# Performance work log

Hardware: AMD Instinct MI355X
Metric: run time of the kernel (lower is better)

The kernel has to match this reference:

```python
import jax, jax.numpy as jnp
import numpy as np

N_NODES = 100000
N_EDGES = 1600000
IN_FEAT = 256
OUT_FEAT = 128


def setup_inputs() -> dict:
    key = jax.random.key(0)
    ks = jax.random.split(key, 8)
    x = jax.random.normal(ks[0], (N_NODES, IN_FEAT), dtype=jnp.float32)
    rows0 = jnp.sort(jax.random.randint(ks[1], (N_EDGES,), 0, N_NODES, dtype=jnp.int32))
    cols0 = jax.random.randint(ks[2], (N_EDGES,), 0, N_NODES, dtype=jnp.int32)
    vals0 = jax.random.uniform(ks[3], (N_EDGES,), dtype=jnp.float32)
    rows1 = jnp.sort(jax.random.randint(ks[4], (N_EDGES,), 0, N_NODES, dtype=jnp.int32))
    cols1 = jax.random.randint(ks[5], (N_EDGES,), 0, N_NODES, dtype=jnp.int32)
    vals1 = jax.random.uniform(ks[6], (N_EDGES,), dtype=jnp.float32)
    kw0, kw1 = jax.random.split(ks[7])
    # glorot-uniform-ish scale for [IN_FEAT, OUT_FEAT]
    limit = float(np.sqrt(6.0 / (IN_FEAT + OUT_FEAT)))
    W0 = jax.random.uniform(kw0, (IN_FEAT, OUT_FEAT), minval=-limit, maxval=limit, dtype=jnp.float32)
    W1 = jax.random.uniform(kw1, (IN_FEAT, OUT_FEAT), minval=-limit, maxval=limit, dtype=jnp.float32)
    return {"x": x, "rows0": rows0, "cols0": cols0, "vals0": vals0,
            "rows1": rows1, "cols1": cols1, "vals1": vals1, "W0": W0, "W1": W1}


def _spmm(rows, cols, vals, dense, n_rows):
    # sparse [N,N] (COO) @ dense [N,D] -> [N,D]
    gathered = vals[:, None] * dense[cols]          # [E, D]
    return jax.ops.segment_sum(gathered, rows, num_segments=n_rows)


def reference(x, rows0, cols0, vals0, rows1, cols1, vals1, W0, W1):
    # GraphConvolution with dropout=0 (identity), featureless=False, no bias, relu.
    # support_i = A_i @ (x @ W_i); output = relu(sum_i support_i)
    s0 = _spmm(rows0, cols0, vals0, x @ W0, N_NODES)
    s1 = _spmm(rows1, cols1, vals1, x @ W1, N_NODES)
    return jax.nn.relu(s0 + s1)
```

## Files before the change

kernel.cpp:

```cpp
#include <hip/hip_runtime.h>
#include <hip/hip_bf16.h>
#include <stdint.h>

#define NN   100000
#define NE   1600000
#define KIN  256
#define FOUT 128

typedef __attribute__((ext_vector_type(8))) short short8;
typedef __attribute__((ext_vector_type(4))) float f32x4;
typedef __attribute__((ext_vector_type(2))) float f32x2;

static __device__ __forceinline__ unsigned short f2bf(float f) {
  unsigned int u = __float_as_uint(f);
  u += 0x7fffu + ((u >> 16) & 1u);
  return (unsigned short)(u >> 16);
}

static __device__ __forceinline__ short8 pack8(float4 u, float4 v) {
  short8 r;
  r[0] = (short)f2bf(u.x); r[1] = (short)f2bf(u.y);
  r[2] = (short)f2bf(u.z); r[3] = (short)f2bf(u.w);
  r[4] = (short)f2bf(v.x); r[5] = (short)f2bf(v.y);
  r[6] = (short)f2bf(v.z); r[7] = (short)f2bf(v.w);
  return r;
}

__global__ void convert_w(const float* __restrict__ W0, const float* __restrict__ W1,
                          unsigned short* __restrict__ wt) {
  int n = blockIdx.x;
  int k = threadIdx.x;
  int which = blockIdx.y;
  const float* W = which ? W1 : W0;
  wt[(size_t)which * (FOUT * KIN) + n * KIN + k] = f2bf(W[k * FOUT + n]);
}

__global__ __launch_bounds__(256) void build_rowptr(const int* __restrict__ rows0,
                                                    const int* __restrict__ rows1,
                                                    int* __restrict__ rp0,
                                                    int* __restrict__ rp1) {
  const int e = blockIdx.x * 256 + threadIdx.x;
  const int* rows = blockIdx.y ? rows1 : rows0;
  int* rp = blockIdx.y ? rp1 : rp0;
  int r1 = rows[e];
  int r2 = (e + 1 < NE) ? rows[e + 1] : NN;
  if (e == 0)
    for (int r = 0; r <= r1; ++r) rp[r] = 0;
  for (int r = r1 + 1; r <= r2; ++r) rp[r] = e + 1;
}

__global__ __launch_bounds__(256) void gemm_fused(const float* __restrict__ x,
                                                  const unsigned short* __restrict__ wt,
                                                  unsigned short* __restrict__ h) {
  const int tid  = threadIdx.x;
  const int lane = tid & 63;
  const int wv   = tid >> 6;
  const int which = wv & 1;
  const int rowbase = blockIdx.x * 64 + (wv >> 1) * 32;
  const int m    = lane & 15;
  const int quad = lane >> 4;

  const unsigned short* w = wt + (size_t)which * (FOUT * KIN);
  unsigned short* hh = h + (size_t)which * NN * FOUT;

  int r0 = rowbase + m;
  int r1 = rowbase + 16 + m;
  int r0c = r0 < NN ? r0 : NN - 1;
  int r1c = r1 < NN ? r1 : NN - 1;
  const float* ap0 = x + (size_t)r0c * KIN + quad * 8;
  const float* ap1 = x + (size_t)r1c * KIN + quad * 8;

  const unsigned short* bp[8];
#pragma unroll
  for (int j = 0; j < 8; ++j)
    bp[j] = w + (size_t)(j * 16 + m) * KIN + quad * 8;

  f32x4 acc[2][8];
#pragma unroll
  for (int i = 0; i < 2; ++i)
#pragma unroll
    for (int j = 0; j < 8; ++j)
      acc[i][j] = (f32x4){0.f, 0.f, 0.f, 0.f};

#pragma unroll
  for (int ki = 0; ki < 8; ++ki) {
    const int ko = ki * 32;
    float4 a0lo = *(const float4*)(ap0 + ko);
    float4 a0hi = *(const float4*)(ap0 + ko + 4);
    float4 a1lo = *(const float4*)(ap1 + ko);
    float4 a1hi = *(const float4*)(ap1 + ko + 4);
    short8 a0 = pack8(a0lo, a0hi);
    short8 a1 = pack8(a1lo, a1hi);
#pragma unroll
    for (int j = 0; j < 8; ++j) {
      short8 b = *(const short8*)(bp[j] + ko);
      acc[0][j] = __builtin_amdgcn_mfma_f32_16x16x32_bf16(a0, b, acc[0][j], 0, 0, 0);
      acc[1][j] = __builtin_amdgcn_mfma_f32_16x16x32_bf16(a1, b, acc[1][j], 0, 0, 0);
    }
  }

#pragma unroll
  for (int i = 0; i < 2; ++i) {
#pragma unroll
    for (int reg = 0; reg < 4; ++reg) {
      int grow = rowbase + i * 16 + quad * 4 + reg;
      if (grow < NN) {
#pragma unroll
        for (int j = 0; j < 8; ++j)
          hh[(size_t)grow * FOUT + j * 16 + m] = f2bf(acc[i][j][reg]);
      }
    }
  }
}

static __device__ __forceinline__ void spmm_row(const int* __restrict__ cols,
                                                const float* __restrict__ vals,
                                                const unsigned short* __restrict__ hsrc,
                                                const int* __restrict__ rp,
                                                int r, int fo,
                                                float& sx, float& sy) {
  int s = __builtin_amdgcn_readfirstlane(rp[r]);
  int e = __builtin_amdgcn_readfirstlane(rp[r + 1]);
  int i = s;
  for (; i + 8 <= e; i += 8) {
    unsigned g[8];
#pragma unroll
    for (int u = 0; u < 8; ++u) {
      int c = cols[i + u];
      g[u] = *(const unsigned*)(hsrc + (size_t)c * FOUT + fo);
    }
#pragma unroll
    for (int u = 0; u < 8; ++u) {
      float v = vals[i + u];
      sx += v * __uint_as_float(g[u] << 16);
      sy += v * __uint_as_float(g[u] & 0xffff0000u);
    }
  }
  for (; i < e; ++i) {
    int c = cols[i];
    float v = vals[i];
    unsigned g = *(const unsigned*)(hsrc + (size_t)c * FOUT + fo);
    sx += v * __uint_as_float(g << 16);
    sy += v * __uint_as_float(g & 0xffff0000u);
  }
}

__global__ __launch_bounds__(256) void spmm_relu(
    const int* __restrict__ rp0, const int* __restrict__ cols0, const float* __restrict__ vals0,
    const int* __restrict__ rp1, const int* __restrict__ cols1, const float* __restrict__ vals1,
    const unsigned short* __restrict__ h, float* __restrict__ out) {
  const int lane = threadIdx.x & 63;
  int r = blockIdx.x * 4 + (threadIdx.x >> 6);
  r = __builtin_amdgcn_readfirstlane(r);
  const int fo = lane * 2;

  const unsigned short* h0 = h;
  const unsigned short* h1 = h + (size_t)NN * FOUT;

  float sx = 0.f, sy = 0.f;
  spmm_row(cols0, vals0, h0, rp0, r, fo, sx, sy);
  spmm_row(cols1, vals1, h1, rp1, r, fo, sx, sy);

  f32x2 o;
  o.x = sx > 0.f ? sx : 0.f;
  o.y = sy > 0.f ? sy : 0.f;
  __builtin_nontemporal_store(o, (f32x2*)(out + (size_t)r * FOUT + fo));
}

extern "C" void kernel_launch(void* const* d_in, const int* in_sizes, int n_in,
                              void* d_out, int out_size, void* d_ws, size_t ws_size,
                              hipStream_t stream) {
  const float* x     = (const float*)d_in[0];
  const int*   rows0 = (const int*)d_in[1];
  const int*   cols0 = (const int*)d_in[2];
  const float* vals0 = (const float*)d_in[3];
  const int*   rows1 = (const int*)d_in[4];
  const int*   cols1 = (const int*)d_in[5];
  const float* vals1 = (const float*)d_in[6];
  const float* W0    = (const float*)d_in[7];
  const float* W1    = (const float*)d_in[8];
  float* out = (float*)d_out;

  char* ws = (char*)d_ws;
  unsigned short* wt = (unsigned short*)(ws);
  unsigned short* h  = (unsigned short*)(ws + 131072);
  int* rp0 = (int*)(ws + 51331072);
  int* rp1 = (int*)(ws + 51731136);

  build_rowptr<<<dim3(6250, 2), 256, 0, stream>>>(rows0, rows1, rp0, rp1);
  convert_w<<<dim3(128, 2), 256, 0, stream>>>(W0, W1, wt);
  gemm_fused<<<(NN + 63) / 64, 256, 0, stream>>>(x, wt, h);
  spmm_relu<<<25000, 256, 0, stream>>>(rp0, cols0, vals0, rp1, cols1, vals1, h, out);
}
```

Before: 393.0 us.

## Split GEMM by weight via grid, stage output in LDS, interleave SpMM gathers

The GEMM now takes the weight index from a second grid dimension. Each wave covers 64 output columns instead of 128, which lowers accumulator register pressure. Its bf16 results are staged through shared memory so that global stores become 16-byte coalesced rows instead of scattered 2-byte writes. The SpMM kernel interleaves gathers from both adjacency matrices, issuing 16 independent loads per iteration to raise memory-level parallelism, with a 4-wide tail loop. The trade-off is that the GEMM reads x twice (once per weight) and uses more shared memory per block.

```diff
diff --git a/kernel.cpp b/kernel.cpp
--- a/kernel.cpp
+++ b/kernel.cpp
@@ -49,14 +49,17 @@
   for (int r = r1 + 1; r <= r2; ++r) rp[r] = e + 1;
 }
 
-__global__ __launch_bounds__(256) void gemm_fused(const float* __restrict__ x,
-                                                  const unsigned short* __restrict__ wt,
-                                                  unsigned short* __restrict__ h) {
+__global__ __launch_bounds__(256) void gemm_mfma(const float* __restrict__ x,
+                                                 const unsigned short* __restrict__ wt,
+                                                 unsigned short* __restrict__ h) {
+  __shared__ __align__(16) unsigned short tile[4][32 * 64];
+
   const int tid  = threadIdx.x;
   const int lane = tid & 63;
   const int wv   = tid >> 6;
-  const int which = wv & 1;
+  const int which = blockIdx.y;
   const int rowbase = blockIdx.x * 64 + (wv >> 1) * 32;
+  const int colbase = (wv & 1) * 64;
   const int m    = lane & 15;
   const int quad = lane >> 4;
 
@@ -69,72 +72,89 @@
   int r1c = r1 < NN ? r1 : NN - 1;
   const float* ap0 = x + (size_t)r0c * KIN + quad * 8;
   const float* ap1 = x + (size_t)r1c * KIN + quad * 8;
-
-  const unsigned short* bp[8];
-#pragma unroll
-  for (int j = 0; j < 8; ++j)
-    bp[j] = w + (size_t)(j * 16 + m) * KIN + quad * 8;
-
-  f32x4 acc[2][8];
+  const unsigned short* b0p = w + (size_t)(colbase + 0  + m) * KIN + quad * 8;
+  const unsigned short* b1p = w + (size_t)(colbase + 16 + m) * KIN + quad * 8;
+  const unsigned short* b2p = w + (size_t)(colbase + 32 + m) * KIN + quad * 8;
+  const unsigned short* b3p = w + (size_t)(colbase + 48 + m) * KIN + quad * 8;
+
+  f32x4 acc[2][4];
 #pragma unroll
   for (int i = 0; i < 2; ++i)
 #pragma unroll
-    for (int j = 0; j < 8; ++j)
+    for (int j = 0; j < 4; ++j)
       acc[i][j] = (f32x4){0.f, 0.f, 0.f, 0.f};
 
-#pragma unroll
-  for (int ki = 0; ki < 8; ++ki) {
-    const int ko = ki * 32;
+#pragma unroll 2
+  for (int ko = 0; ko < KIN; ko += 32) {
     float4 a0lo = *(const float4*)(ap0 + ko);
     float4 a0hi = *(const float4*)(ap0 + ko + 4);
     float4 a1lo = *(const float4*)(ap1 + ko);
     float4 a1hi = *(const float4*)(ap1 + ko + 4);
+    short8 b0 = *(const short8*)(b0p + ko);
+    short8 b1 = *(const short8*)(b1p + ko);
+    short8 b2 = *(const short8*)(b2p + ko);
+    short8 b3 = *(const short8*)(b3p + ko);
     short8 a0 = pack8(a0lo, a0hi);
     short8 a1 = pack8(a1lo, a1hi);
-#pragma unroll
-    for (int j = 0; j < 8; ++j) {
-      short8 b = *(const short8*)(bp[j] + ko);
-      acc[0][j] = __builtin_amdgcn_mfma_f32_16x16x32_bf16(a0, b, acc[0][j], 0, 0, 0);
-      acc[1][j] = __builtin_amdgcn_mfma_f32_16x16x32_bf16(a1, b, acc[1][j], 0, 0, 0);
-    }
-  }
-
-#pragma unroll
-  for (int i = 0; i < 2; ++i) {
-#pragma unroll
-    for (int reg = 0; reg < 4; ++reg) {
-      int grow = rowbase + i * 16 + quad * 4 + reg;
-      if (grow < NN) {
-#pragma unroll
-        for (int j = 0; j < 8; ++j)
-          hh[(size_t)grow * FOUT + j * 16 + m] = f2bf(acc[i][j][reg]);
-      }
-    }
-  }
-}
-
-static __device__ __forceinline__ void spmm_row(const int* __restrict__ cols,
-                                                const float* __restrict__ vals,
-                                                const unsigned short* __restrict__ hsrc,
-                                                const int* __restrict__ rp,
-                                                int r, int fo,
-                                                float& sx, float& sy) {
-  int s = __builtin_amdgcn_readfirstlane(rp[r]);
-  int e = __builtin_amdgcn_readfirstlane(rp[r + 1]);
-  int i = s;
-  for (; i + 8 <= e; i += 8) {
-    unsigned g[8];
-#pragma unroll
-    for (int u = 0; u < 8; ++u) {
-      int c = cols[i + u];
-      g[u] = *(const unsigned*)(hsrc + (size_t)c * FOUT + fo);
-    }
-#pragma unroll
-    for (int u = 0; u < 8; ++u) {
-      float v = vals[i + u];
-      sx += v * __uint_as_float(g[u] << 16);
-      sy += v * __uint_as_float(g[u] & 0xffff0000u);
-    }
+    acc[0][0] = __builtin_amdgcn_mfma_f32_16x16x32_bf16(a0, b0, acc[0][0], 0, 0, 0);
+    acc[0][1] = __builtin_amdgcn_mfma_f32_16x16x32_bf16(a0, b1, acc[0][1], 0, 0, 0);
+    acc[0][2] = __builtin_amdgcn_mfma_f32_16x16x32_bf16(a0, b2, acc[0][2], 0, 0, 0);
+    acc[0][3] = __builtin_amdgcn_mfma_f32_16x16x32_bf16(a0, b3, acc[0][3], 0, 0, 0);
+    acc[1][0] = __builtin_amdgcn_mfma_f32_16x16x32_bf16(a1, b0, acc[1][0], 0, 0, 0);
+    acc[1][1] = __builtin_amdgcn_mfma_f32_16x16x32_bf16(a1, b1, acc[1][1], 0, 0, 0);
+    acc[1][2] = __builtin_amdgcn_mfma_f32_16x16x32_bf16(a1, b2, acc[1][2], 0, 0, 0);
+    acc[1][3] = __builtin_amdgcn_mfma_f32_16x16x32_bf16(a1, b3, acc[1][3], 0, 0, 0);
+  }
+
+#pragma unroll
+  for (int i = 0; i < 2; ++i)
+#pragma unroll
+    for (int reg = 0; reg < 4; ++reg)
+#pragma unroll
+      for (int j = 0; j < 4; ++j)
+        tile[wv][(i * 16 + quad * 4 + reg) * 64 + j * 16 + m] = f2bf(acc[i][j][reg]);
+
+#pragma unroll
+  for (int p = 0; p < 4; ++p) {
+    int row = p * 8 + (lane >> 3);
+    int colb = (lane & 7) * 8;
+    uint4 v = *(const uint4*)&tile[wv][row * 64 + colb];
+    int grow = rowbase + row;
+    if (grow < NN)
+      *(uint4*)&hh[(size_t)grow * FOUT + colbase + colb] = v;
+  }
+}
+
+static __device__ __forceinline__ void consume8(const float* __restrict__ vals, int i,
+                                                const unsigned* g, float& sx, float& sy) {
+#pragma unroll
+  for (int u = 0; u < 8; ++u) {
+    float v = vals[i + u];
+    sx += v * __uint_as_float(g[u] << 16);
+    sy += v * __uint_as_float(g[u] & 0xffff0000u);
+  }
+}
+
+static __device__ __forceinline__ void tail_spmm(const int* __restrict__ cols,
+                                                 const float* __restrict__ vals,
+                                                 const unsigned short* __restrict__ hsrc,
+                                                 int i, int e, int fo,
+                                                 float& sx, float& sy) {
+  for (; i + 4 <= e; i += 4) {
+    int c0 = cols[i], c1 = cols[i + 1], c2 = cols[i + 2], c3 = cols[i + 3];
+    unsigned g0 = *(const unsigned*)(hsrc + (size_t)c0 * FOUT + fo);
+    unsigned g1 = *(const unsigned*)(hsrc + (size_t)c1 * FOUT + fo);
+    unsigned g2 = *(const unsigned*)(hsrc + (size_t)c2 * FOUT + fo);
+    unsigned g3 = *(const unsigned*)(hsrc + (size_t)c3 * FOUT + fo);
+    float v0 = vals[i], v1 = vals[i + 1], v2 = vals[i + 2], v3 = vals[i + 3];
+    sx += v0 * __uint_as_float(g0 << 16);
+    sy += v0 * __uint_as_float(g0 & 0xffff0000u);
+    sx += v1 * __uint_as_float(g1 << 16);
+    sy += v1 * __uint_as_float(g1 & 0xffff0000u);
+    sx += v2 * __uint_as_float(g2 << 16);
+    sy += v2 * __uint_as_float(g2 & 0xffff0000u);
+    sx += v3 * __uint_as_float(g3 << 16);
+    sy += v3 * __uint_as_float(g3 & 0xffff0000u);
   }
   for (; i < e; ++i) {
     int c = cols[i];
@@ -157,9 +177,32 @@
   const unsigned short* h0 = h;
   const unsigned short* h1 = h + (size_t)NN * FOUT;
 
+  int i0 = __builtin_amdgcn_readfirstlane(rp0[r]);
+  int e0 = __builtin_amdgcn_readfirstlane(rp0[r + 1]);
+  int i1 = __builtin_amdgcn_readfirstlane(rp1[r]);
+  int e1 = __builtin_amdgcn_readfirstlane(rp1[r + 1]);
+
   float sx = 0.f, sy = 0.f;
-  spmm_row(cols0, vals0, h0, rp0, r, fo, sx, sy);
-  spmm_row(cols1, vals1, h1, rp1, r, fo, sx, sy);
+
+  while (i0 + 8 <= e0 && i1 + 8 <= e1) {
+    unsigned g0[8], g1[8];
+#pragma unroll
+    for (int u = 0; u < 8; ++u) {
+      int c = cols0[i0 + u];
+      g0[u] = *(const unsigned*)(h0 + (size_t)c * FOUT + fo);
+    }
+#pragma unroll
+    for (int u = 0; u < 8; ++u) {
+      int c = cols1[i1 + u];
+      g1[u] = *(const unsigned*)(h1 + (size_t)c * FOUT + fo);
+    }
+    consume8(vals0, i0, g0, sx, sy);
+    consume8(vals1, i1, g1, sx, sy);
+    i0 += 8;
+    i1 += 8;
+  }
+  tail_spmm(cols0, vals0, h0, i0, e0, fo, sx, sy);
+  tail_spmm(cols1, vals1, h1, i1, e1, fo, sx, sy);
 
   f32x2 o;
   o.x = sx > 0.f ? sx : 0.f;
@@ -189,6 +232,6 @@
 
   build_rowptr<<<dim3(6250, 2), 256, 0, stream>>>(rows0, rows1, rp0, rp1);
   convert_w<<<dim3(128, 2), 256, 0, stream>>>(W0, W1, wt);
-  gemm_fused<<<(NN + 63) / 64, 256, 0, stream>>>(x, wt, h);
+  gemm_mfma<<<dim3((NN + 63) / 64, 2), 256, 0, stream>>>(x, wt, h);
   spmm_relu<<<25000, 256, 0, stream>>>(rp0, cols0, vals0, rp1, cols1, vals1, h, out);
 }
```

New measurement: 386.2 us. About the same (-1.7%).
